# Optimization experiments

Hardware: AMD Instinct MI355X
Metric: run time of the kernel (lower is better)

## Reference

```python
import jax, jax.numpy as jnp
import numpy as np

B, D, E, H, C = 16384, 512, 16, 2048, 1
LN_EPS = 1e-5


def setup_inputs() -> dict:
    key = jax.random.key(0)
    ks = jax.random.split(key, 6)
    scale = 0.02
    return {
        "z": jax.random.normal(ks[0], (B, D), jnp.float32),
        "gate_w": jax.random.normal(ks[1], (D, E), jnp.float32) * scale,
        "gate_b": jnp.zeros((E,), jnp.float32),
        "ln_scale": jnp.ones((E, D), jnp.float32),
        "ln_bias": jnp.zeros((E, D), jnp.float32),
        "w1": jax.random.normal(ks[2], (E, D, H), jnp.float32) * scale,
        "b1": jnp.zeros((E, H), jnp.float32),
        "w2": jax.random.normal(ks[3], (E, H, C), jnp.float32) * scale,
        "b2": jnp.zeros((E, C), jnp.float32),
    }


def reference(z, gate_w, gate_b, ln_scale, ln_bias, w1, b1, w2, b2):
    # Gate: softmax over experts, top-1 routing by argmax
    g = jax.nn.softmax(z @ gate_w + gate_b, axis=-1)  # (B, E)
    idx = jnp.argmax(g, axis=-1)                      # (B,)

    # LayerNorm statistics are expert-independent (affine differs per expert)
    mu = jnp.mean(z, axis=-1, keepdims=True)
    var = jnp.mean(jnp.square(z - mu), axis=-1, keepdims=True)
    zn = (z - mu) / jnp.sqrt(var + LN_EPS)            # (B, D)

    # Loop over the small fixed expert set; combine by top-1 mask.
    logits = jnp.zeros((z.shape[0],), z.dtype)
    for e in range(E):
        x = zn * ln_scale[e] + ln_bias[e]                       # (B, D)
        h = jax.nn.gelu(x @ w1[e] + b1[e], approximate=False)   # (B, H)
        o = jnp.squeeze(h @ w2[e] + b2[e], axis=-1)             # (B,) since C==1
        logits = jnp.where(idx == e, o, logits)
    return logits, g
```

## Files before the change

### kernel.cpp

```cpp
#include <hip/hip_runtime.h>
#include <math.h>

#define NB 16384
#define ND 512
#define NE 16
#define NH 2048
#define BM 128
#define BN 128
#define BK 64
#define NCH (NH / BN)
#define NTB 8
#define NPW (NCH * 2)
#define LN_EPS 1e-5f

typedef __attribute__((ext_vector_type(8))) short s8v;
typedef __attribute__((ext_vector_type(4))) float f4v;

#define WS_W1T_OFF   ((size_t)0)
#define WS_W1T_BYTES ((size_t)NE * NH * ND * 2)
#define WS_XN_OFF    (WS_W1T_OFF + WS_W1T_BYTES)
#define WS_XN_BYTES  ((size_t)NB * ND * 2)
#define WS_XNS_OFF   (WS_XN_OFF + WS_XN_BYTES)
#define WS_XNS_BYTES ((size_t)NB * ND * 2)
#define WS_PART_OFF  (WS_XNS_OFF + WS_XNS_BYTES)
#define WS_PART_BYTES ((size_t)NB * NPW * 4)
#define WS_IDX_OFF   (WS_PART_OFF + WS_PART_BYTES)
#define WS_ROWOF_OFF (WS_IDX_OFF + (size_t)NB * 4)
#define WS_CNT_OFF   (WS_ROWOF_OFF + (size_t)NB * 4)
#define WS_ROWS_OFF  (WS_CNT_OFF + 256)

__device__ __forceinline__ unsigned short bf16_rne(float f) {
    unsigned u = __float_as_uint(f);
    unsigned r = (u + 0x7fffu + ((u >> 16) & 1u)) >> 16;
    return (unsigned short)r;
}

__global__ __launch_bounds__(256) void w1conv_kernel(
    const float* __restrict__ w1, unsigned short* __restrict__ w1t)
{
    int bid = blockIdx.x;
    int e = bid & 15;
    int rest = bid >> 4;
    int db = rest & 7;
    int hb = rest >> 3;
    int h = hb * 256 + threadIdx.x;

    const float* src = w1 + ((size_t)e * ND + db * 64) * NH + h;
    unsigned int u[32];
#pragma unroll
    for (int p = 0; p < 32; ++p) {
        float f0 = src[(size_t)(2 * p) * NH];
        float f1 = src[(size_t)(2 * p + 1) * NH];
        u[p] = (unsigned)bf16_rne(f0) | ((unsigned)bf16_rne(f1) << 16);
    }
    uint4* dst = reinterpret_cast<uint4*>(
        w1t + ((size_t)e * NH + h) * ND + db * 64);
#pragma unroll
    for (int p = 0; p < 8; ++p)
        dst[p] = make_uint4(u[4 * p], u[4 * p + 1], u[4 * p + 2], u[4 * p + 3]);
}

__global__ __launch_bounds__(256) void gate_ln_kernel(
    const float* __restrict__ z, const float* __restrict__ gw,
    const float* __restrict__ gb, const float* __restrict__ ln_s,
    const float* __restrict__ ln_b, unsigned short* __restrict__ xn,
    int* __restrict__ idx_ws, float* __restrict__ g_out)
{
    int wave = threadIdx.x >> 6;
    int lane = threadIdx.x & 63;
    int b = blockIdx.x * 4 + wave;
    int q = lane & 3, dg = lane >> 2;

    const float* zr = z + (size_t)b * ND;
    float4 zv[8];
#pragma unroll
    for (int i = 0; i < 8; ++i)
        zv[i] = *reinterpret_cast<const float4*>(zr + dg * 32 + i * 4);

    float sum = 0.f, ssq = 0.f;
    float ga[4] = {0.f, 0.f, 0.f, 0.f};
#pragma unroll
    for (int i = 0; i < 8; ++i) {
        float zs[4] = {zv[i].x, zv[i].y, zv[i].z, zv[i].w};
#pragma unroll
        for (int t = 0; t < 4; ++t) {
            int d = dg * 32 + i * 4 + t;
            float4 w4 = *reinterpret_cast<const float4*>(gw + (size_t)d * NE + q * 4);
            ga[0] = fmaf(zs[t], w4.x, ga[0]);
            ga[1] = fmaf(zs[t], w4.y, ga[1]);
            ga[2] = fmaf(zs[t], w4.z, ga[2]);
            ga[3] = fmaf(zs[t], w4.w, ga[3]);
            sum += zs[t];
            ssq = fmaf(zs[t], zs[t], ssq);
        }
    }
#pragma unroll
    for (int m = 4; m <= 32; m <<= 1) {
        sum += __shfl_xor(sum, m);
        ssq += __shfl_xor(ssq, m);
#pragma unroll
        for (int j = 0; j < 4; ++j) ga[j] += __shfl_xor(ga[j], m);
    }
#pragma unroll
    for (int j = 0; j < 4; ++j) ga[j] += gb[q * 4 + j];

    float mu = sum * (1.f / ND);
    float var = ssq * (1.f / ND) - mu * mu;
    float rstd = rsqrtf(var + LN_EPS);

    float lmax = fmaxf(fmaxf(ga[0], ga[1]), fmaxf(ga[2], ga[3]));
    lmax = fmaxf(lmax, __shfl_xor(lmax, 1));
    lmax = fmaxf(lmax, __shfl_xor(lmax, 2));
    float ge[4], lsum = 0.f;
#pragma unroll
    for (int j = 0; j < 4; ++j) { ge[j] = __expf(ga[j] - lmax); lsum += ge[j]; }
    lsum += __shfl_xor(lsum, 1);
    lsum += __shfl_xor(lsum, 2);
    float rden = 1.f / lsum;

    int li = 1000;
#pragma unroll
    for (int j = 3; j >= 0; --j) if (ga[j] == lmax) li = q * 4 + j;
    li = min(li, __shfl_xor(li, 1));
    li = min(li, __shfl_xor(li, 2));

    float gv0 = ge[0] * rden, gv1 = ge[1] * rden;
    float gv2 = ge[2] * rden, gv3 = ge[3] * rden;
    int srcl = lane >> 2;
    float t0 = __shfl(gv0, srcl), t1 = __shfl(gv1, srcl);
    float t2 = __shfl(gv2, srcl), t3 = __shfl(gv3, srcl);
    float gval = (q == 0) ? t0 : (q == 1) ? t1 : (q == 2) ? t2 : t3;
    if (lane < NE) g_out[(size_t)b * NE + lane] = gval;

    float4 xa, xc;
    if (q == 0)      { xa = zv[0]; xc = zv[1]; }
    else if (q == 1) { xa = zv[2]; xc = zv[3]; }
    else if (q == 2) { xa = zv[4]; xc = zv[5]; }
    else             { xa = zv[6]; xc = zv[7]; }
    int dofs = dg * 32 + q * 8;
    const float* ls = ln_s + (size_t)li * ND + dofs;
    const float* lb = ln_b + (size_t)li * ND + dofs;
    float4 s0 = *reinterpret_cast<const float4*>(ls);
    float4 s1 = *reinterpret_cast<const float4*>(ls + 4);
    float4 u0 = *reinterpret_cast<const float4*>(lb);
    float4 u1 = *reinterpret_cast<const float4*>(lb + 4);
    unsigned short xb[8];
    xb[0] = bf16_rne((xa.x - mu) * rstd * s0.x + u0.x);
    xb[1] = bf16_rne((xa.y - mu) * rstd * s0.y + u0.y);
    xb[2] = bf16_rne((xa.z - mu) * rstd * s0.z + u0.z);
    xb[3] = bf16_rne((xa.w - mu) * rstd * s0.w + u0.w);
    xb[4] = bf16_rne((xc.x - mu) * rstd * s1.x + u1.x);
    xb[5] = bf16_rne((xc.y - mu) * rstd * s1.y + u1.y);
    xb[6] = bf16_rne((xc.z - mu) * rstd * s1.z + u1.z);
    xb[7] = bf16_rne((xc.w - mu) * rstd * s1.w + u1.w);
    *reinterpret_cast<s8v*>(xn + (size_t)b * ND + dofs) =
        *reinterpret_cast<s8v*>(xb);

    if (lane == 0) idx_ws[b] = li;
}

__global__ __launch_bounds__(256) void bucket_kernel(
    const int* __restrict__ idx_ws, int* __restrict__ counts,
    int* __restrict__ rows)
{
    __shared__ int qc[4];
    int e = blockIdx.x;
    int tid = threadIdx.x, w = tid >> 6, lane = tid & 63;
    const int4* p = reinterpret_cast<const int4*>(idx_ws) + (size_t)w * 1024;

    int c = 0;
#pragma unroll 4
    for (int it = 0; it < 16; ++it) {
        int4 v = p[it * 64 + lane];
        c += (v.x == e) + (v.y == e) + (v.z == e) + (v.w == e);
    }
#pragma unroll
    for (int m = 1; m < 64; m <<= 1) c += __shfl_xor(c, m);
    if (lane == 0) qc[w] = c;
    __syncthreads();

    int base = 0;
    for (int j = 0; j < w; ++j) base += qc[j];
    unsigned long long below = (lane == 0) ? 0ull : ((~0ull) >> (64 - lane));
    int* re = rows + (size_t)e * NB;
    int run = base;
#pragma unroll 2
    for (int it = 0; it < 16; ++it) {
        int4 v = p[it * 64 + lane];
        int vv[4] = {v.x, v.y, v.z, v.w};
#pragma unroll
        for (int k = 0; k < 4; ++k) {
            unsigned long long m = __ballot(vv[k] == e);
            if (vv[k] == e)
                re[run + __popcll(m & below)] = w * 4096 + (it * 64 + lane) * 4 + k;
            run += __popcll(m);
        }
    }
    if (tid == 0) counts[e] = qc[0] + qc[1] + qc[2] + qc[3];
}

__global__ __launch_bounds__(256) void gather_kernel(
    const unsigned short* __restrict__ xn, const int* __restrict__ counts,
    const int* __restrict__ rows, unsigned short* __restrict__ xns,
    int* __restrict__ rowof)
{
    int wave = threadIdx.x >> 6, lane = threadIdx.x & 63;
    int slot = blockIdx.x * 4 + wave;

    int pfx = 0, e = 0;
#pragma unroll
    for (int i = 0; i < NE; ++i) {
        int c = counts[i];
        if (e == i && slot >= pfx + c) { pfx += c; e = i + 1; }
    }
    int row = rows[(size_t)e * NB + (slot - pfx)];
    s8v v = *reinterpret_cast<const s8v*>(xn + (size_t)row * ND + lane * 8);
    *reinterpret_cast<s8v*>(xns + (size_t)slot * ND + lane * 8) = v;
    if (lane == 0) rowof[slot] = row;
}

__global__ __launch_bounds__(256, 3) void mfma_mlp(
    const unsigned short* __restrict__ xns, const unsigned short* __restrict__ w1t,
    const float* __restrict__ b1, const float* __restrict__ w2,
    const int* __restrict__ counts, float* __restrict__ part)
{
    __shared__ unsigned short A_lds[BM * BK];
    __shared__ unsigned short B_lds[BN * BK];

    int bid = blockIdx.x;
    int e = bid & 15;
    int rest = bid >> 4;
    int ch = rest & 15;
    int tb0 = rest >> 4;
    int c0 = ch * BN;
    int tid = threadIdx.x, lane = tid & 63, wave = tid >> 6;
    int wm = wave & 1, wn = wave >> 1;

    int cnt = counts[e];
    int pfx = 0;
    for (int i = 0; i < e; ++i) pfx += counts[i];

    int rquad = lane >> 3;
    int sbyte = ((lane & 7) * 16) ^ (rquad << 4);

    const char* xb = (const char*)xns;
    const char* wb = (const char*)w1t;

    unsigned boff32[4];
#pragma unroll
    for (int i = 0; i < 4; ++i) {
        int cl = (wave * 4 + i) * 8 + rquad;
        boff32[i] = (unsigned)((e * NH + c0 + cl) * 1024) + sbyte;
    }

    int g = lane >> 4;
    int fr = lane & 15;
    int sw = (lane & 7) << 4;
    int kb0 = (g * 16) ^ sw, kb1 = (64 + g * 16) ^ sw;
    int aoffs[4], boffs[4];
#pragma unroll
    for (int f = 0; f < 4; ++f) {
        aoffs[f] = (wm * 64 + f * 16 + fr) * 128;
        boffs[f] = (wn * 64 + f * 16 + fr) * 128;
    }

    for (int tb = tb0; tb * BM < cnt; tb += NTB) {
        int rbase = tb * BM;
        int sbase = pfx + rbase;

        unsigned aoff32[4];
#pragma unroll
        for (int i = 0; i < 4; ++i) {
            int rloc = (wave * 4 + i) * 8 + rquad;
            int slot = min(sbase + rloc, NB - 1);
            aoff32[i] = (unsigned)(slot * 1024) + sbyte;
        }

        f4v acc[4][4];
#pragma unroll
        for (int rf = 0; rf < 4; ++rf)
#pragma unroll
            for (int cf = 0; cf < 4; ++cf) acc[rf][cf] = (f4v){0.f, 0.f, 0.f, 0.f};

#pragma unroll
        for (int ss = 0; ss < 8; ++ss) {
            __syncthreads();
#pragma unroll
            for (int i = 0; i < 4; ++i) {
                __builtin_amdgcn_global_load_lds(
                    (const __attribute__((address_space(1))) void*)
                        (xb + aoff32[i] + ss * 128),
                    (__attribute__((address_space(3))) void*)
                        &A_lds[(wave * 4 + i) * 8 * BK], 16, 0, 0);
                __builtin_amdgcn_global_load_lds(
                    (const __attribute__((address_space(1))) void*)
                        (wb + boff32[i] + ss * 128),
                    (__attribute__((address_space(3))) void*)
                        &B_lds[(wave * 4 + i) * 8 * BK], 16, 0, 0);
            }
            __syncthreads();

#pragma unroll
            for (int ks = 0; ks < 2; ++ks) {
                int kb = ks ? kb1 : kb0;
                s8v a[4], bb[4];
#pragma unroll
                for (int rf = 0; rf < 4; ++rf)
                    a[rf] = *reinterpret_cast<const s8v*>(
                        (const char*)A_lds + aoffs[rf] + kb);
#pragma unroll
                for (int cf = 0; cf < 4; ++cf)
                    bb[cf] = *reinterpret_cast<const s8v*>(
                        (const char*)B_lds + boffs[cf] + kb);
#pragma unroll
                for (int rf = 0; rf < 4; ++rf)
#pragma unroll
                    for (int cf = 0; cf < 4; ++cf)
                        acc[rf][cf] = __builtin_amdgcn_mfma_f32_16x16x32_bf16(
                            a[rf], bb[cf], acc[rf][cf], 0, 0, 0);
            }
        }

        float b1v[4], w2v[4];
#pragma unroll
        for (int cf = 0; cf < 4; ++cf) {
            int col = c0 + wn * 64 + cf * 16 + fr;
            b1v[cf] = b1[(size_t)e * NH + col];
            w2v[cf] = w2[(size_t)e * NH + col];
        }
#pragma unroll
        for (int rf = 0; rf < 4; ++rf) {
            float pj[4] = {0.f, 0.f, 0.f, 0.f};
#pragma unroll
            for (int cf = 0; cf < 4; ++cf) {
#pragma unroll
                for (int j = 0; j < 4; ++j) {
                    float h = acc[rf][cf][j] + b1v[cf];
                    float uu = h * (0.7978845608f + 0.0356774081f * h * h);
                    float ex = __expf(2.f * uu);
                    float th = 1.f - 2.f / (ex + 1.f);
                    pj[j] = fmaf(0.5f * h * (1.f + th), w2v[cf], pj[j]);
                }
            }
#pragma unroll
            for (int m = 1; m < 16; m <<= 1)
#pragma unroll
                for (int j = 0; j < 4; ++j) pj[j] += __shfl_xor(pj[j], m);
            if ((lane & 15) == 0) {
#pragma unroll
                for (int j = 0; j < 4; ++j) {
                    int rloc = wm * 64 + rf * 16 + g * 4 + j;
                    if (rbase + rloc < cnt)
                        part[(size_t)(sbase + rloc) * NPW + ch * 2 + wn] = pj[j];
                }
            }
        }
    }
}

__global__ __launch_bounds__(256) void finalize_kernel(
    const float* __restrict__ part, const int* __restrict__ rowof,
    const int* __restrict__ idx_ws, const float* __restrict__ b2,
    float* __restrict__ logits)
{
    int s = blockIdx.x * 256 + threadIdx.x;
    const f4v* p = reinterpret_cast<const f4v*>(part + (size_t)s * NPW);
    float sum = 0.f;
#pragma unroll
    for (int i = 0; i < 8; ++i) {
        f4v v = p[i];
        sum += (v[0] + v[1]) + (v[2] + v[3]);
    }
    int row = rowof[s];
    logits[row] = sum + b2[idx_ws[row]];
}

extern "C" void kernel_launch(void* const* d_in, const int* in_sizes, int n_in,
                              void* d_out, int out_size, void* d_ws, size_t ws_size,
                              hipStream_t stream) {
    const float* z    = (const float*)d_in[0];
    const float* gw   = (const float*)d_in[1];
    const float* gb   = (const float*)d_in[2];
    const float* ln_s = (const float*)d_in[3];
    const float* ln_b = (const float*)d_in[4];
    const float* w1   = (const float*)d_in[5];
    const float* b1   = (const float*)d_in[6];
    const float* w2   = (const float*)d_in[7];
    const float* b2   = (const float*)d_in[8];

    float* logits = (float*)d_out;
    float* g_out  = (float*)d_out + NB;

    char* ws = (char*)d_ws;
    unsigned short* w1t = (unsigned short*)(ws + WS_W1T_OFF);
    unsigned short* xn  = (unsigned short*)(ws + WS_XN_OFF);
    unsigned short* xns = (unsigned short*)(ws + WS_XNS_OFF);
    float* part  = (float*)(ws + WS_PART_OFF);
    int* idx_ws  = (int*)(ws + WS_IDX_OFF);
    int* rowof   = (int*)(ws + WS_ROWOF_OFF);
    int* cnts    = (int*)(ws + WS_CNT_OFF);
    int* rowl    = (int*)(ws + WS_ROWS_OFF);

    w1conv_kernel<<<NE * 64, 256, 0, stream>>>(w1, w1t);
    gate_ln_kernel<<<NB / 4, 256, 0, stream>>>(z, gw, gb, ln_s, ln_b,
                                               xn, idx_ws, g_out);
    bucket_kernel<<<NE, 256, 0, stream>>>(idx_ws, cnts, rowl);
    gather_kernel<<<NB / 4, 256, 0, stream>>>(xn, cnts, rowl, xns, rowof);
    mfma_mlp<<<NE * NCH * NTB, 256, 0, stream>>>(xns, w1t, b1, w2, cnts, part);
    finalize_kernel<<<NB / 256, 256, 0, stream>>>(part, rowof, idx_ws, b2,
                                                  logits);
}
```

Baseline: 155.5 us.

## Merge w1 conversion into gate kernel, reorder expert blocks, use rational tanh

```diff
diff --git a/kernel.cpp b/kernel.cpp
--- a/kernel.cpp
+++ b/kernel.cpp
@@ -9,7 +9,6 @@
 #define BN 128
 #define BK 64
 #define NCH (NH / BN)
-#define NTB 8
 #define NPW (NCH * 2)
 #define LN_EPS 1e-5f
 
@@ -35,37 +34,37 @@
     return (unsigned short)r;
 }
 
-__global__ __launch_bounds__(256) void w1conv_kernel(
-    const float* __restrict__ w1, unsigned short* __restrict__ w1t)
-{
-    int bid = blockIdx.x;
-    int e = bid & 15;
-    int rest = bid >> 4;
-    int db = rest & 7;
-    int hb = rest >> 3;
-    int h = hb * 256 + threadIdx.x;
-
-    const float* src = w1 + ((size_t)e * ND + db * 64) * NH + h;
-    unsigned int u[32];
-#pragma unroll
-    for (int p = 0; p < 32; ++p) {
-        float f0 = src[(size_t)(2 * p) * NH];
-        float f1 = src[(size_t)(2 * p + 1) * NH];
-        u[p] = (unsigned)bf16_rne(f0) | ((unsigned)bf16_rne(f1) << 16);
-    }
-    uint4* dst = reinterpret_cast<uint4*>(
-        w1t + ((size_t)e * NH + h) * ND + db * 64);
-#pragma unroll
-    for (int p = 0; p < 8; ++p)
-        dst[p] = make_uint4(u[4 * p], u[4 * p + 1], u[4 * p + 2], u[4 * p + 3]);
-}
-
-__global__ __launch_bounds__(256) void gate_ln_kernel(
+__global__ __launch_bounds__(256) void gate_w1_kernel(
     const float* __restrict__ z, const float* __restrict__ gw,
     const float* __restrict__ gb, const float* __restrict__ ln_s,
-    const float* __restrict__ ln_b, unsigned short* __restrict__ xn,
+    const float* __restrict__ ln_b, const float* __restrict__ w1,
+    unsigned short* __restrict__ w1t, unsigned short* __restrict__ xn,
     int* __restrict__ idx_ws, float* __restrict__ g_out)
 {
+    if (blockIdx.x >= NB / 4) {
+        int bid = blockIdx.x - NB / 4;
+        int e = bid & 15;
+        int rest = bid >> 4;
+        int db = rest & 7;
+        int hb = rest >> 3;
+        int h = hb * 256 + threadIdx.x;
+
+        const float* src = w1 + ((size_t)e * ND + db * 64) * NH + h;
+        unsigned int u[32];
+#pragma unroll
+        for (int p = 0; p < 32; ++p) {
+            float f0 = src[(size_t)(2 * p) * NH];
+            float f1 = src[(size_t)(2 * p + 1) * NH];
+            u[p] = (unsigned)bf16_rne(f0) | ((unsigned)bf16_rne(f1) << 16);
+        }
+        uint4* dst = reinterpret_cast<uint4*>(
+            w1t + ((size_t)e * NH + h) * ND + db * 64);
+#pragma unroll
+        for (int p = 0; p < 8; ++p)
+            dst[p] = make_uint4(u[4 * p], u[4 * p + 1], u[4 * p + 2], u[4 * p + 3]);
+        return;
+    }
+
     int wave = threadIdx.x >> 6;
     int lane = threadIdx.x & 63;
     int b = blockIdx.x * 4 + wave;
@@ -228,8 +227,9 @@
     __shared__ unsigned short B_lds[BN * BK];
 
     int bid = blockIdx.x;
-    int e = bid & 15;
-    int rest = bid >> 4;
+    int phase = bid >> 10;
+    int e = (bid & 7) + phase * 8;
+    int rest = (bid >> 3) & 127;
     int ch = rest & 15;
     int tb0 = rest >> 4;
     int c0 = ch * BN;
@@ -264,7 +264,7 @@
         boffs[f] = (wn * 64 + f * 16 + fr) * 128;
     }
 
-    for (int tb = tb0; tb * BM < cnt; tb += NTB) {
+    for (int tb = tb0; tb * BM < cnt; tb += 8) {
         int rbase = tb * BM;
         int sbase = pfx + rbase;
 
@@ -336,10 +336,13 @@
 #pragma unroll
                 for (int j = 0; j < 4; ++j) {
                     float h = acc[rf][cf][j] + b1v[cf];
-                    float uu = h * (0.7978845608f + 0.0356774081f * h * h);
-                    float ex = __expf(2.f * uu);
-                    float th = 1.f - 2.f / (ex + 1.f);
-                    pj[j] = fmaf(0.5f * h * (1.f + th), w2v[cf], pj[j]);
+                    float u = 0.7978845608f * h * fmaf(0.044715f * h, h, 1.0f);
+                    float u2 = u * u;
+                    float num = u * fmaf(u2, fmaf(u2, 1.0f, 105.0f), 945.0f);
+                    float den = fmaf(u2, fmaf(u2, 15.0f, 420.0f), 945.0f);
+                    float t = num * __builtin_amdgcn_rcpf(den);
+                    t = fminf(fmaxf(t, -1.0f), 1.0f);
+                    pj[j] = fmaf(0.5f * h * (1.0f + t), w2v[cf], pj[j]);
                 }
             }
 #pragma unroll
@@ -401,12 +404,11 @@
     int* cnts    = (int*)(ws + WS_CNT_OFF);
     int* rowl    = (int*)(ws + WS_ROWS_OFF);
 
-    w1conv_kernel<<<NE * 64, 256, 0, stream>>>(w1, w1t);
-    gate_ln_kernel<<<NB / 4, 256, 0, stream>>>(z, gw, gb, ln_s, ln_b,
-                                               xn, idx_ws, g_out);
+    gate_w1_kernel<<<NB / 4 + NE * 64, 256, 0, stream>>>(
+        z, gw, gb, ln_s, ln_b, w1, w1t, xn, idx_ws, g_out);
     bucket_kernel<<<NE, 256, 0, stream>>>(idx_ws, cnts, rowl);
     gather_kernel<<<NB / 4, 256, 0, stream>>>(xn, cnts, rowl, xns, rowof);
-    mfma_mlp<<<NE * NCH * NTB, 256, 0, stream>>>(xns, w1t, b1, w2, cnts, part);
+    mfma_mlp<<<2048, 256, 0, stream>>>(xns, w1t, b1, w2, cnts, part);
     finalize_kernel<<<NB / 256, 256, 0, stream>>>(part, rowof, idx_ws, b2,
                                                   logits);
 }
```

Result: faster. 142.5 us (-8.4%).
